# Kernel tuning notes

Hardware: AMD Instinct MI355X
Metric: run time of the kernel (lower is better)

Reference implementation:

```python
import jax, jax.numpy as jnp
import numpy as np

NUM_NODES = 100000
HIDDEN = 128
NUM_EDGES = 625000


def setup_inputs() -> dict:
    key = jax.random.key(0)
    k_emb, k_edge = jax.random.split(key)
    node_ids = jnp.arange(NUM_NODES, dtype=jnp.int64 if jax.config.jax_enable_x64 else jnp.int32)
    edge_index = jax.random.randint(k_edge, (2, NUM_EDGES), 0, NUM_NODES, dtype=jnp.int32)
    emb_weight = jax.random.normal(k_emb, (NUM_NODES, HIDDEN), dtype=jnp.float32)
    return {"node_ids": node_ids, "edge_index": edge_index, "emb_weight": emb_weight}


def reference(node_ids, edge_index, emb_weight):
    # sources = node_ids[edge_index[0]]; vs = emb[sources]  -> [E, H] gather
    sources = node_ids[edge_index[0]]
    vs = emb_weight[sources]  # [E, H]
    tgt = edge_index[1]
    # scatter_mean over dim 0: segment-sum then divide by per-target counts
    sums = jax.ops.segment_sum(vs, tgt, num_segments=NUM_NODES)  # [N, H]
    counts = jax.ops.segment_sum(jnp.ones((vs.shape[0],), dtype=vs.dtype), tgt,
                                 num_segments=NUM_NODES)  # [N]
    # empty segments -> 0 (matches torch_scatter scatter_mean)
    return sums / jnp.maximum(counts, 1.0)[:, None]
```

## Files before the change

kernel.cpp:

```cpp
#include <hip/hip_runtime.h>


#define NUM_NODES 100000
#define HIDDEN    128
#define NUM_EDGES 625000
#define CAP       32

#define NBINS     391
#define BIN_NODES 256
#define BIN_SHIFT 8
#define BIN_ECAP  2048
#define LSTRIDE   33

#define EPA_THREAD 8
#define ABLOCK_E   (256 * EPA_THREAD)
#define ABLOCKS    ((NUM_EDGES + ABLOCK_E - 1) / ABLOCK_E)

#define CAST_BLOCKS 3125

typedef float vfloat4 __attribute__((ext_vector_type(4)));

__device__ __forceinline__ unsigned bf16_rne(float f) {
    unsigned x = __float_as_uint(f);
    return (x + 0x7FFFu + ((x >> 16) & 1u)) >> 16;
}

__device__ __forceinline__ unsigned pack2(float lo, float hi) {
    return bf16_rne(lo) | (bf16_rne(hi) << 16);
}

__global__ __launch_bounds__(256) void bin_kernel(
    const int* __restrict__ node_ids,
    const int* __restrict__ src,
    const int* __restrict__ tgt,
    int* __restrict__ cursor,
    uint2* __restrict__ part)
{
    __shared__ int hist[NBINS];
    __shared__ int basearr[NBINS];
    int tid = threadIdx.x, bid = blockIdx.x;
    for (int i = tid; i < NBINS; i += 256) hist[i] = 0;
    __syncthreads();

    int t[EPA_THREAD], nid[EPA_THREAD];
#pragma unroll
    for (int k = 0; k < EPA_THREAD; ++k) {
        int e = bid * ABLOCK_E + k * 256 + tid;
        bool ok = e < NUM_EDGES;
        t[k]   = ok ? tgt[e] : -1;
        nid[k] = node_ids[ok ? src[e] : 0];
    }
#pragma unroll
    for (int k = 0; k < EPA_THREAD; ++k)
        if (t[k] >= 0) atomicAdd(&hist[t[k] >> BIN_SHIFT], 1);
    __syncthreads();

    for (int i = tid; i < NBINS; i += 256) {
        int c = hist[i];
        basearr[i] = (c > 0) ? atomicAdd(&cursor[i], c) : 0;
        hist[i] = 0;
    }
    __syncthreads();

#pragma unroll
    for (int k = 0; k < EPA_THREAD; ++k) {
        if (t[k] < 0) continue;
        int b = t[k] >> BIN_SHIFT;
        int r = atomicAdd(&hist[b], 1);
        int off = basearr[b] + r;
        if (off < BIN_ECAP)
            part[(size_t)b * BIN_ECAP + off] =
                make_uint2((unsigned)nid[k], (unsigned)t[k]);
    }
}

__global__ __launch_bounds__(256) void binbucket_kernel(
    const uint2* __restrict__ part, const int* __restrict__ cursor,
    int* __restrict__ cnt,
    int* __restrict__ buckets)
{
    __shared__ int lcnt[BIN_NODES];
    __shared__ int lbuck[BIN_NODES * LSTRIDE];
    int tid = threadIdx.x, b = blockIdx.x;

    lcnt[tid] = 0;
    __syncthreads();

    int n = cursor[b];
    if (n > BIN_ECAP) n = BIN_ECAP;
    const uint2* p = part + (size_t)b * BIN_ECAP;
    for (int i = tid; i < n; i += 256) {
        uint2 e = p[i];
        int local = (int)(e.y & (BIN_NODES - 1));
        int pos = atomicAdd(&lcnt[local], 1);
        if (pos < CAP)
            lbuck[local * LSTRIDE + pos] = (int)e.x;
    }
    __syncthreads();

    int node = b * BIN_NODES + tid;
    if (node < NUM_NODES) cnt[node] = lcnt[tid];

    int* gb = buckets + (size_t)b * (BIN_NODES * CAP);
    for (int i = tid; i < BIN_NODES * CAP; i += 256)
        gb[i] = lbuck[(i >> 5) * LSTRIDE + (i & 31)];
}

__global__ __launch_bounds__(256) void cast_kernel(
    const float* __restrict__ emb,
    uint4* __restrict__ emb16)
{
    int j = blockIdx.x * 256 + threadIdx.x;
    const vfloat4* ev = reinterpret_cast<const vfloat4*>(emb);
    vfloat4 a = __builtin_nontemporal_load(ev + j * 4 + 0);
    vfloat4 b = __builtin_nontemporal_load(ev + j * 4 + 1);
    vfloat4 c = __builtin_nontemporal_load(ev + j * 4 + 2);
    vfloat4 d = __builtin_nontemporal_load(ev + j * 4 + 3);
    uint4 o0, o1;
    o0.x = pack2(a.x, a.y); o0.y = pack2(a.z, a.w);
    o0.z = pack2(b.x, b.y); o0.w = pack2(b.z, b.w);
    o1.x = pack2(c.x, c.y); o1.y = pack2(c.z, c.w);
    o1.z = pack2(d.x, d.y); o1.w = pack2(d.z, d.w);
    emb16[j * 2 + 0] = o0;
    emb16[j * 2 + 1] = o1;
}

__global__ __launch_bounds__(256) void gather_kernel(
    const int* __restrict__ cnt, const int* __restrict__ buckets,
    const uint4* __restrict__ emb16, float* __restrict__ out)
{
    int gid  = blockIdx.x * blockDim.x + threadIdx.x;
    int n    = gid >> 4;
    int lane = gid & 15;
    if (n >= NUM_NODES) return;

    int c = cnt[n];
    int m = (c < CAP) ? c : CAP;
    const int* b = buckets + n * CAP;

    float acc[8] = {0,0,0,0,0,0,0,0};
    auto accum = [&](uint4 u) {
        acc[0] += __uint_as_float(u.x << 16);
        acc[1] += __uint_as_float(u.x & 0xFFFF0000u);
        acc[2] += __uint_as_float(u.y << 16);
        acc[3] += __uint_as_float(u.y & 0xFFFF0000u);
        acc[4] += __uint_as_float(u.z << 16);
        acc[5] += __uint_as_float(u.z & 0xFFFF0000u);
        acc[6] += __uint_as_float(u.w << 16);
        acc[7] += __uint_as_float(u.w & 0xFFFF0000u);
    };

    int i = 0;
    for (; i + 3 < m; i += 4) {
        int4 s = *reinterpret_cast<const int4*>(b + i);
        uint4 u0 = emb16[(size_t)s.x * 16 + lane];
        uint4 u1 = emb16[(size_t)s.y * 16 + lane];
        uint4 u2 = emb16[(size_t)s.z * 16 + lane];
        uint4 u3 = emb16[(size_t)s.w * 16 + lane];
        accum(u0); accum(u1); accum(u2); accum(u3);
    }
    for (; i < m; ++i) {
        uint4 u = emb16[(size_t)b[i] * 16 + lane];
        accum(u);
    }

    float inv = (c > 0) ? 1.0f / (float)c : 0.0f;
    vfloat4 r0, r1;
    r0.x = acc[0] * inv; r0.y = acc[1] * inv; r0.z = acc[2] * inv; r0.w = acc[3] * inv;
    r1.x = acc[4] * inv; r1.y = acc[5] * inv; r1.z = acc[6] * inv; r1.w = acc[7] * inv;
    float* o = out + (size_t)n * HIDDEN + lane * 8;
    __builtin_nontemporal_store(r0, reinterpret_cast<vfloat4*>(o));
    __builtin_nontemporal_store(r1, reinterpret_cast<vfloat4*>(o + 4));
}

extern "C" void kernel_launch(void* const* d_in, const int* in_sizes, int n_in,
                              void* d_out, int out_size, void* d_ws, size_t ws_size,
                              hipStream_t stream) {
    const int*   node_ids = (const int*)d_in[0];
    const int*   edge_idx = (const int*)d_in[1];
    const float* emb      = (const float*)d_in[2];
    float*       out      = (float*)d_out;

    const int* edge_src = edge_idx;
    const int* edge_tgt = edge_idx + NUM_EDGES;

    char* ws = (char*)d_ws;
    int*   cursor  = (int*)(ws + 0);
    int*   cnt     = (int*)(ws + 4096);
    int*   buckets = (int*)(ws + 405504);
    uint4* emb16   = (uint4*)(ws + 13250560);
    uint2* part    = (uint2*)(ws + 13250560);

    (void)hipMemsetAsync(cursor, 0, NBINS * sizeof(int), stream);

    bin_kernel<<<ABLOCKS, 256, 0, stream>>>(node_ids, edge_src, edge_tgt,
                                            cursor, part);
    binbucket_kernel<<<NBINS, 256, 0, stream>>>(part, cursor, cnt, buckets);
    cast_kernel<<<CAST_BLOCKS, 256, 0, stream>>>(emb, emb16);
    {
        long long total = (long long)NUM_NODES * 16;
        int grid = (int)((total + 255) / 256);
        gather_kernel<<<grid, 256, 0, stream>>>(cnt, buckets, emb16, out);
    }
}
```

Before: 168.6 us.

## Fuse binning with cast and bucket build with gather into two kernels

Replaces the four-kernel pipeline (memset, global-atomic binning, per-bin bucketing, cast, gather) with two kernels. The prep kernel bins edges into fixed per-block, per-bin slots and casts embeddings to bf16 in the same launch, which removes the global cursor atomics and the memset. The gather kernel builds node buckets in shared memory and reduces them directly, which removes the bucket round-trip through global memory. The costs are only 391 gather blocks of 1024 threads, which may underfill the GPU and serialise four nodes per thread group. Any block that puts more than 24 edges into one bin would also drop edges, which makes it a capacity assumption about the input distribution.

```diff
diff --git a/kernel.cpp b/kernel.cpp
--- a/kernel.cpp
+++ b/kernel.cpp
@@ -9,7 +9,7 @@
 #define NBINS     391
 #define BIN_NODES 256
 #define BIN_SHIFT 8
-#define BIN_ECAP  2048
+#define SLOT_CAP  24
 #define LSTRIDE   33
 
 #define EPA_THREAD 8
@@ -17,6 +17,7 @@
 #define ABLOCKS    ((NUM_EDGES + ABLOCK_E - 1) / ABLOCK_E)
 
 #define CAST_BLOCKS 3125
+#define PREP_BLOCKS (ABLOCKS + CAST_BLOCKS)
 
 typedef float vfloat4 __attribute__((ext_vector_type(4)));
 
@@ -29,116 +30,99 @@
     return bf16_rne(lo) | (bf16_rne(hi) << 16);
 }
 
-__global__ __launch_bounds__(256) void bin_kernel(
+__global__ __launch_bounds__(256) void prep_kernel(
     const int* __restrict__ node_ids,
     const int* __restrict__ src,
     const int* __restrict__ tgt,
-    int* __restrict__ cursor,
-    uint2* __restrict__ part)
+    const float* __restrict__ emb,
+    int* __restrict__ blkcnt,
+    unsigned* __restrict__ part,
+    uint4* __restrict__ emb16)
 {
-    __shared__ int hist[NBINS];
-    __shared__ int basearr[NBINS];
-    int tid = threadIdx.x, bid = blockIdx.x;
-    for (int i = tid; i < NBINS; i += 256) hist[i] = 0;
-    __syncthreads();
+    int bid = blockIdx.x;
+    int tid = threadIdx.x;
 
-    int t[EPA_THREAD], nid[EPA_THREAD];
+    if (bid < ABLOCKS) {
+        __shared__ int hist[NBINS];
+        for (int i = tid; i < NBINS; i += 256) hist[i] = 0;
+        __syncthreads();
+
+        int t[EPA_THREAD], nid[EPA_THREAD];
 #pragma unroll
-    for (int k = 0; k < EPA_THREAD; ++k) {
-        int e = bid * ABLOCK_E + k * 256 + tid;
-        bool ok = e < NUM_EDGES;
-        t[k]   = ok ? tgt[e] : -1;
-        nid[k] = node_ids[ok ? src[e] : 0];
+        for (int k = 0; k < EPA_THREAD; ++k) {
+            int e = bid * ABLOCK_E + k * 256 + tid;
+            bool ok = e < NUM_EDGES;
+            t[k]   = ok ? tgt[e] : -1;
+            nid[k] = node_ids[ok ? src[e] : 0];
+        }
+#pragma unroll
+        for (int k = 0; k < EPA_THREAD; ++k) {
+            if (t[k] < 0) continue;
+            int b = t[k] >> BIN_SHIFT;
+            int r = atomicAdd(&hist[b], 1);
+            if (r < SLOT_CAP)
+                part[((size_t)b * ABLOCKS + bid) * SLOT_CAP + r] =
+                    (unsigned)nid[k] |
+                    ((unsigned)(t[k] & (BIN_NODES - 1)) << 17);
+        }
+        __syncthreads();
+        for (int i = tid; i < NBINS; i += 256)
+            blkcnt[bid * NBINS + i] = hist[i];
+    } else {
+        int j = (bid - ABLOCKS) * 256 + tid;
+        const vfloat4* ev = reinterpret_cast<const vfloat4*>(emb);
+        vfloat4 a = __builtin_nontemporal_load(ev + j * 4 + 0);
+        vfloat4 b = __builtin_nontemporal_load(ev + j * 4 + 1);
+        vfloat4 c = __builtin_nontemporal_load(ev + j * 4 + 2);
+        vfloat4 d = __builtin_nontemporal_load(ev + j * 4 + 3);
+        uint4 o0, o1;
+        o0.x = pack2(a.x, a.y); o0.y = pack2(a.z, a.w);
+        o0.z = pack2(b.x, b.y); o0.w = pack2(b.z, b.w);
+        o1.x = pack2(c.x, c.y); o1.y = pack2(c.z, c.w);
+        o1.z = pack2(d.x, d.y); o1.w = pack2(d.z, d.w);
+        emb16[j * 2 + 0] = o0;
+        emb16[j * 2 + 1] = o1;
     }
-#pragma unroll
-    for (int k = 0; k < EPA_THREAD; ++k)
-        if (t[k] >= 0) atomicAdd(&hist[t[k] >> BIN_SHIFT], 1);
-    __syncthreads();
+}
 
-    for (int i = tid; i < NBINS; i += 256) {
-        int c = hist[i];
-        basearr[i] = (c > 0) ? atomicAdd(&cursor[i], c) : 0;
-        hist[i] = 0;
+__global__ __launch_bounds__(1024) void gather_kernel(
+    const unsigned* __restrict__ part,
+    const int* __restrict__ blkcnt,
+    const uint4* __restrict__ emb16,
+    float* __restrict__ out)
+{
+    __shared__ int lcnt[BIN_NODES];
+    __shared__ int lbuck[BIN_NODES * LSTRIDE];
+    __shared__ int sblk[ABLOCKS];
+
+    int tid = threadIdx.x, b = blockIdx.x;
+
+    if (tid < BIN_NODES) lcnt[tid] = 0;
+    for (int i = tid; i < ABLOCKS; i += 1024) {
+        int c = blkcnt[i * NBINS + b];
+        sblk[i] = (c < SLOT_CAP) ? c : SLOT_CAP;
     }
     __syncthreads();
 
-#pragma unroll
-    for (int k = 0; k < EPA_THREAD; ++k) {
-        if (t[k] < 0) continue;
-        int b = t[k] >> BIN_SHIFT;
-        int r = atomicAdd(&hist[b], 1);
-        int off = basearr[b] + r;
-        if (off < BIN_ECAP)
-            part[(size_t)b * BIN_ECAP + off] =
-                make_uint2((unsigned)nid[k], (unsigned)t[k]);
-    }
-}
-
-__global__ __launch_bounds__(256) void binbucket_kernel(
-    const uint2* __restrict__ part, const int* __restrict__ cursor,
-    int* __restrict__ cnt,
-    int* __restrict__ buckets)
-{
-    __shared__ int lcnt[BIN_NODES];
-    __shared__ int lbuck[BIN_NODES * LSTRIDE];
-    int tid = threadIdx.x, b = blockIdx.x;
-
-    lcnt[tid] = 0;
-    __syncthreads();
-
-    int n = cursor[b];
-    if (n > BIN_ECAP) n = BIN_ECAP;
-    const uint2* p = part + (size_t)b * BIN_ECAP;
-    for (int i = tid; i < n; i += 256) {
-        uint2 e = p[i];
-        int local = (int)(e.y & (BIN_NODES - 1));
-        int pos = atomicAdd(&lcnt[local], 1);
-        if (pos < CAP)
-            lbuck[local * LSTRIDE + pos] = (int)e.x;
+    const unsigned* pb = part + (size_t)b * ABLOCKS * SLOT_CAP;
+    const int total_slots = ABLOCKS * SLOT_CAP;
+    for (int s = tid; s < total_slots; s += 1024) {
+        int blk  = s / SLOT_CAP;
+        int slot = s - blk * SLOT_CAP;
+        if (slot < sblk[blk]) {
+            unsigned v = pb[s];
+            int local = (int)(v >> 17);
+            int pos = atomicAdd(&lcnt[local], 1);
+            if (pos < CAP)
+                lbuck[local * LSTRIDE + pos] = (int)(v & 0x1FFFFu);
+        }
     }
     __syncthreads();
 
-    int node = b * BIN_NODES + tid;
-    if (node < NUM_NODES) cnt[node] = lcnt[tid];
+    int lane = tid & 15;
+    int grp  = tid >> 4;
 
-    int* gb = buckets + (size_t)b * (BIN_NODES * CAP);
-    for (int i = tid; i < BIN_NODES * CAP; i += 256)
-        gb[i] = lbuck[(i >> 5) * LSTRIDE + (i & 31)];
-}
-
-__global__ __launch_bounds__(256) void cast_kernel(
-    const float* __restrict__ emb,
-    uint4* __restrict__ emb16)
-{
-    int j = blockIdx.x * 256 + threadIdx.x;
-    const vfloat4* ev = reinterpret_cast<const vfloat4*>(emb);
-    vfloat4 a = __builtin_nontemporal_load(ev + j * 4 + 0);
-    vfloat4 b = __builtin_nontemporal_load(ev + j * 4 + 1);
-    vfloat4 c = __builtin_nontemporal_load(ev + j * 4 + 2);
-    vfloat4 d = __builtin_nontemporal_load(ev + j * 4 + 3);
-    uint4 o0, o1;
-    o0.x = pack2(a.x, a.y); o0.y = pack2(a.z, a.w);
-    o0.z = pack2(b.x, b.y); o0.w = pack2(b.z, b.w);
-    o1.x = pack2(c.x, c.y); o1.y = pack2(c.z, c.w);
-    o1.z = pack2(d.x, d.y); o1.w = pack2(d.z, d.w);
-    emb16[j * 2 + 0] = o0;
-    emb16[j * 2 + 1] = o1;
-}
-
-__global__ __launch_bounds__(256) void gather_kernel(
-    const int* __restrict__ cnt, const int* __restrict__ buckets,
-    const uint4* __restrict__ emb16, float* __restrict__ out)
-{
-    int gid  = blockIdx.x * blockDim.x + threadIdx.x;
-    int n    = gid >> 4;
-    int lane = gid & 15;
-    if (n >= NUM_NODES) return;
-
-    int c = cnt[n];
-    int m = (c < CAP) ? c : CAP;
-    const int* b = buckets + n * CAP;
-
-    float acc[8] = {0,0,0,0,0,0,0,0};
+    float acc[8];
     auto accum = [&](uint4 u) {
         acc[0] += __uint_as_float(u.x << 16);
         acc[1] += __uint_as_float(u.x & 0xFFFF0000u);
@@ -150,27 +134,43 @@
         acc[7] += __uint_as_float(u.w & 0xFFFF0000u);
     };
 
-    int i = 0;
-    for (; i + 3 < m; i += 4) {
-        int4 s = *reinterpret_cast<const int4*>(b + i);
-        uint4 u0 = emb16[(size_t)s.x * 16 + lane];
-        uint4 u1 = emb16[(size_t)s.y * 16 + lane];
-        uint4 u2 = emb16[(size_t)s.z * 16 + lane];
-        uint4 u3 = emb16[(size_t)s.w * 16 + lane];
-        accum(u0); accum(u1); accum(u2); accum(u3);
+#pragma unroll
+    for (int it = 0; it < 4; ++it) {
+        int nl = it * 64 + grp;
+        int n  = b * BIN_NODES + nl;
+        if (n >= NUM_NODES) continue;
+        int c = lcnt[nl];
+        int m = (c < CAP) ? c : CAP;
+        const int* bl = lbuck + nl * LSTRIDE;
+
+#pragma unroll 8
+        for (int q = 0; q < 8; ++q) acc[q] = 0.f;
+
+        int i = 0;
+        for (; i + 3 < m; i += 4) {
+            int s0 = bl[i + 0], s1 = bl[i + 1];
+            int s2 = bl[i + 2], s3 = bl[i + 3];
+            uint4 u0 = emb16[(size_t)s0 * 16 + lane];
+            uint4 u1 = emb16[(size_t)s1 * 16 + lane];
+            uint4 u2 = emb16[(size_t)s2 * 16 + lane];
+            uint4 u3 = emb16[(size_t)s3 * 16 + lane];
+            accum(u0); accum(u1); accum(u2); accum(u3);
+        }
+        for (; i < m; ++i) {
+            uint4 u = emb16[(size_t)bl[i] * 16 + lane];
+            accum(u);
+        }
+
+        float inv = (c > 0) ? 1.0f / (float)c : 0.0f;
+        vfloat4 r0, r1;
+        r0.x = acc[0] * inv; r0.y = acc[1] * inv;
+        r0.z = acc[2] * inv; r0.w = acc[3] * inv;
+        r1.x = acc[4] * inv; r1.y = acc[5] * inv;
+        r1.z = acc[6] * inv; r1.w = acc[7] * inv;
+        float* o = out + (size_t)n * HIDDEN + lane * 8;
+        __builtin_nontemporal_store(r0, reinterpret_cast<vfloat4*>(o));
+        __builtin_nontemporal_store(r1, reinterpret_cast<vfloat4*>(o + 4));
     }
-    for (; i < m; ++i) {
-        uint4 u = emb16[(size_t)b[i] * 16 + lane];
-        accum(u);
-    }
-
-    float inv = (c > 0) ? 1.0f / (float)c : 0.0f;
-    vfloat4 r0, r1;
-    r0.x = acc[0] * inv; r0.y = acc[1] * inv; r0.z = acc[2] * inv; r0.w = acc[3] * inv;
-    r1.x = acc[4] * inv; r1.y = acc[5] * inv; r1.z = acc[6] * inv; r1.w = acc[7] * inv;
-    float* o = out + (size_t)n * HIDDEN + lane * 8;
-    __builtin_nontemporal_store(r0, reinterpret_cast<vfloat4*>(o));
-    __builtin_nontemporal_store(r1, reinterpret_cast<vfloat4*>(o + 4));
 }
 
 extern "C" void kernel_launch(void* const* d_in, const int* in_sizes, int n_in,
@@ -185,21 +185,11 @@
     const int* edge_tgt = edge_idx + NUM_EDGES;
 
     char* ws = (char*)d_ws;
-    int*   cursor  = (int*)(ws + 0);
-    int*   cnt     = (int*)(ws + 4096);
-    int*   buckets = (int*)(ws + 405504);
-    uint4* emb16   = (uint4*)(ws + 13250560);
-    uint2* part    = (uint2*)(ws + 13250560);
+    int*      blkcnt = (int*)(ws + 0);
+    unsigned* part   = (unsigned*)(ws + 480000);
+    uint4*    emb16  = (uint4*)(ws + 11966080);
 
-    (void)hipMemsetAsync(cursor, 0, NBINS * sizeof(int), stream);
-
-    bin_kernel<<<ABLOCKS, 256, 0, stream>>>(node_ids, edge_src, edge_tgt,
-                                            cursor, part);
-    binbucket_kernel<<<NBINS, 256, 0, stream>>>(part, cursor, cnt, buckets);
-    cast_kernel<<<CAST_BLOCKS, 256, 0, stream>>>(emb, emb16);
-    {
-        long long total = (long long)NUM_NODES * 16;
-        int grid = (int)((total + 255) / 256);
-        gather_kernel<<<grid, 256, 0, stream>>>(cnt, buckets, emb16, out);
-    }
+    prep_kernel<<<PREP_BLOCKS, 256, 0, stream>>>(node_ids, edge_src, edge_tgt,
+                                                 emb, blkcnt, part, emb16);
+    gather_kernel<<<NBINS, 1024, 0, stream>>>(part, blkcnt, emb16, out);
 }
```

New measurement: 158.7 us. 5.9% less time.
